# Kernel optimization log

Hardware: AMD Instinct MI355X
Metric: run time of the kernel (lower is better)

Reference implementation:

```python
import jax, jax.numpy as jnp
import numpy as np

SCALE = 8      # scale_factor from map_to_mat_info
PATCH = 32     # up_delta - low_delta + 1 == right_delta - left_delta + 1 (uniform interior patches)


def setup_inputs() -> dict:
    key = jax.random.key(0)
    mat_h, mat_w = 160, 160
    H = (mat_h - 1) * SCALE + PATCH  # 1304: deltas (0,31,0,31) -> no border clipping
    W = (mat_w - 1) * SCALE + PATCH
    x = jax.random.normal(key, (1, 3, H, W), dtype=jnp.float32)
    rgb_weight = jnp.array([0.299, 0.587, 0.114], dtype=jnp.float32).reshape(1, 3, 1, 1)
    return {"x": x, "rgb_weight": rgb_weight, "mat_h": mat_h, "mat_w": mat_w}


def reference(x, rgb_weight, mat_h, mat_w):
    P = PATCH
    # RGB -> grayscale (convert_gray branch for in_channels == 3)
    gray = jnp.sum(x * rgb_weight, axis=1)[0]  # (H, W)
    # Gather all overlapping PxP patches at stride SCALE -> (mat_h, mat_w, P, P)
    rows = (jnp.arange(mat_h) * SCALE)[:, None] + jnp.arange(P)[None, :]  # (mat_h, P)
    cols = (jnp.arange(mat_w) * SCALE)[:, None] + jnp.arange(P)[None, :]  # (mat_w, P)
    p = gray[rows.reshape(-1)].reshape(mat_h, P, -1)              # (mat_h, P, W)
    p = p[:, :, cols.reshape(-1)].reshape(mat_h, P, mat_w, P)     # (mat_h, P, mat_w, P)
    patches = jnp.transpose(p, (0, 2, 1, 3))                      # (mat_h, mat_w, P, P)
    # torch.rfft(signal_ndim=2, onesided=False) == full 2D FFT; power = re^2 + im^2
    F = jnp.fft.fft2(patches)
    log_power = jnp.log(F.real * F.real + F.imag * F.imag + 1.0)
    # High-frequency region sums (h == w == P, static)
    lo = P // 2 - P // 4 - 1   # 7
    up = P // 2 + P // 4       # 24
    r1 = jnp.sum(log_power[..., lo:up + 1, :], axis=(-2, -1))
    r2 = jnp.sum(log_power[..., up + 1:, lo:up + 1], axis=(-2, -1))
    r3 = jnp.sum(log_power[..., :lo, lo:up + 1], axis=(-2, -1))
    mat = (r1 + r2 + r3)[None, None]  # (1, 1, mat_h, mat_w)
    return mat / jnp.max(mat)
```

## Files before the change

### kernel.cpp

```cpp
#include <hip/hip_runtime.h>
#include <math.h>

#define SCALE 8
#define PSZ 32

__device__ constexpr float C32[16] = {
     1.000000000000000f,  0.980785280403230f,  0.923879532511287f,  0.831469612302545f,
     0.707106781186548f,  0.555570233019602f,  0.382683432365090f,  0.195090322016128f,
     0.000000000000000f, -0.195090322016128f, -0.382683432365090f, -0.555570233019602f,
    -0.707106781186548f, -0.831469612302545f, -0.923879532511287f, -0.980785280403230f };
__device__ constexpr float S32[16] = {
     0.000000000000000f,  0.195090322016128f,  0.382683432365090f,  0.555570233019602f,
     0.707106781186548f,  0.831469612302545f,  0.923879532511287f,  0.980785280403230f,
     1.000000000000000f,  0.980785280403230f,  0.923879532511287f,  0.831469612302545f,
     0.707106781186548f,  0.555570233019602f,  0.382683432365090f,  0.195090322016128f };

__device__ __forceinline__ constexpr int brev5(int i) {
    return ((i & 1) << 4) | ((i & 2) << 2) | (i & 4) | ((i & 8) >> 2) | ((i & 16) >> 4);
}

__device__ __forceinline__ void fft32(float re[PSZ], float im[PSZ]) {
#pragma unroll
    for (int i = 0; i < 32; ++i) {
        const int j = brev5(i);
        if (j > i) {
            float t = re[i]; re[i] = re[j]; re[j] = t;
            t = im[i]; im[i] = im[j]; im[j] = t;
        }
    }
#pragma unroll
    for (int s = 1; s <= 5; ++s) {
        const int m = 1 << s;
        const int h = m >> 1;
        const int tstep = 32 >> s;
#pragma unroll
        for (int k = 0; k < 32; k += m) {
#pragma unroll
            for (int j = 0; j < h; ++j) {
                const float wr = C32[j * tstep];
                const float wi = -S32[j * tstep];
                const int a = k + j;
                const int b = k + j + h;
                const float tr = wr * re[b] - wi * im[b];
                const float ti = wr * im[b] + wi * re[b];
                re[b] = re[a] - tr; im[b] = im[a] - ti;
                re[a] = re[a] + tr; im[a] = im[a] + ti;
            }
        }
    }
}

__device__ __forceinline__ unsigned pack_bf2(float hi, float lo) {
    const unsigned uh = __float_as_uint(hi) + 0x8000u;
    const unsigned ul = __float_as_uint(lo) + 0x8000u;
    return (uh & 0xFFFF0000u) | (ul >> 16);
}
__device__ __forceinline__ float bf_hi(unsigned u) { return __uint_as_float(u & 0xFFFF0000u); }
__device__ __forceinline__ float bf_lo(unsigned u) { return __uint_as_float(u << 16); }

__global__ __launch_bounds__(256) void gray_kernel(
        const float* __restrict__ x, const float* __restrict__ w,
        float* __restrict__ g, int n4, long long HW) {
    const int i = blockIdx.x * 256 + threadIdx.x;
    if (i >= n4) return;
    const float w0 = w[0], w1 = w[1], w2 = w[2];
    const float4 a = reinterpret_cast<const float4*>(x)[i];
    const float4 b = reinterpret_cast<const float4*>(x + HW)[i];
    const float4 c = reinterpret_cast<const float4*>(x + 2 * HW)[i];
    float4 o;
    o.x = w0 * a.x + w1 * b.x + w2 * c.x;
    o.y = w0 * a.y + w1 * b.y + w2 * c.y;
    o.z = w0 * a.z + w1 * b.z + w2 * c.z;
    o.w = w0 * a.w + w1 * b.w + w2 * c.w;
    reinterpret_cast<float4*>(g)[i] = o;
}

template <bool GRAY_PRE>
__global__ __launch_bounds__(64) void hfdft_patch_kernel(
        const float* __restrict__ x, const float* __restrict__ w,
        float* __restrict__ out, int H, int W, int mat_h, int mat_w) {
    __shared__ unsigned cb[4 * 528];

    const int lane = threadIdx.x;
    const int total = mat_h * mat_w;
    const long long HW = (long long)H * W;

    {
        const int g = lane >> 5, r = lane & 31;
        int pA = blockIdx.x * 4 + 2 * g;
        if (pA > total - 1) pA = total - 1;
        int pB = pA + 1; if (pB > total - 1) pB = total - 1;
        const int phA = pA / mat_w, pwA = pA % mat_w;
        const int phB = pB / mat_w, pwB = pB % mat_w;
        const bool adj = (phA == phB) && (pwB == pwA + 1);

        float re[PSZ], im[PSZ];
        if (GRAY_PRE) {
            if (adj) {
                const int base = (phA * SCALE + r) * W + pwA * SCALE;
                const float4* g4 = reinterpret_cast<const float4*>(x + base);
                float win[40];
#pragma unroll
                for (int q = 0; q < 10; ++q) {
                    const float4 v = g4[q];
                    win[4 * q + 0] = v.x; win[4 * q + 1] = v.y;
                    win[4 * q + 2] = v.z; win[4 * q + 3] = v.w;
                }
#pragma unroll
                for (int i = 0; i < PSZ; ++i) { re[i] = win[i]; im[i] = win[i + 8]; }
            } else {
                const int baseA = (phA * SCALE + r) * W + pwA * SCALE;
                const int baseB = (phB * SCALE + r) * W + pwB * SCALE;
#pragma unroll
                for (int i = 0; i < PSZ; ++i) { re[i] = x[baseA + i]; im[i] = x[baseB + i]; }
            }
        } else {
            const float w0 = w[0], w1 = w[1], w2 = w[2];
            if (adj && ((W & 3) == 0)) {
                const int base = (phA * SCALE + r) * W + pwA * SCALE;
                const float4* a4 = reinterpret_cast<const float4*>(x + base);
                const float4* b4 = reinterpret_cast<const float4*>(x + HW + base);
                const float4* c4 = reinterpret_cast<const float4*>(x + 2 * HW + base);
                float win[40];
#pragma unroll
                for (int q = 0; q < 10; ++q) {
                    const float4 a = a4[q], b = b4[q], c = c4[q];
                    win[4 * q + 0] = w0 * a.x + w1 * b.x + w2 * c.x;
                    win[4 * q + 1] = w0 * a.y + w1 * b.y + w2 * c.y;
                    win[4 * q + 2] = w0 * a.z + w1 * b.z + w2 * c.z;
                    win[4 * q + 3] = w0 * a.w + w1 * b.w + w2 * c.w;
                }
#pragma unroll
                for (int i = 0; i < PSZ; ++i) { re[i] = win[i]; im[i] = win[i + 8]; }
            } else {
                const int baseA = (phA * SCALE + r) * W + pwA * SCALE;
                const int baseB = (phB * SCALE + r) * W + pwB * SCALE;
#pragma unroll
                for (int i = 0; i < PSZ; ++i) {
                    re[i] = w0 * x[baseA + i] + w1 * x[HW + baseA + i] + w2 * x[2 * HW + baseA + i];
                    im[i] = w0 * x[baseB + i] + w1 * x[HW + baseB + i] + w2 * x[2 * HW + baseB + i];
                }
            }
        }

        fft32(re, im);

        unsigned* cbA = cb + (2 * g) * 528;
        unsigned* cbB = cbA + 528;
        cbA[r] = pack_bf2(re[0], re[16]);
        cbB[r] = pack_bf2(im[0], im[16]);
#pragma unroll
        for (int k = 1; k <= 15; ++k) {
            const int m = 32 - k;
            const float far_ = 0.5f * (re[k] + re[m]);
            const float fai_ = 0.5f * (im[k] - im[m]);
            const float fbr_ = 0.5f * (im[k] + im[m]);
            const float fbi_ = 0.5f * (re[m] - re[k]);
            cbA[k * 33 + r] = pack_bf2(far_, fai_);
            cbB[k * 33 + r] = pack_bf2(fbr_, fbi_);
        }
    }

    __syncthreads();

    {
        const int pl = lane >> 4, slot = lane & 15;
        const int p = blockIdx.x * 4 + pl;
        const unsigned* cbp = cb + pl * 528 + slot * 33;

        float cre[PSZ], cim[PSZ];
#pragma unroll
        for (int r2 = 0; r2 < PSZ; ++r2) {
            const unsigned u = cbp[r2];
            cre[r2] = bf_hi(u);
            cim[r2] = bf_lo(u);
        }

        fft32(cre, cim);

        float s0 = 0.0f, s1 = 0.0f;
        if (slot == 0) {
#pragma unroll
            for (int kr = 0; kr <= 16; ++kr) {
                const int m = (32 - kr) & 31;
                const float g0r = 0.5f * (cre[kr] + cre[m]);
                const float g0i = 0.5f * (cim[kr] - cim[m]);
                const float g1r = 0.5f * (cim[kr] + cim[m]);
                const float g1i = 0.5f * (cre[m] - cre[kr]);
                const float w0c = (kr >= 7 ? 1.0f : 0.0f) + ((kr >= 8 && kr <= 15) ? 1.0f : 0.0f);
                const float w16c = 1.0f + ((kr >= 1 && kr <= 15) ? 1.0f : 0.0f);
                if (w0c > 0.0f)
                    s0 = fmaf(w0c, __logf(g0r * g0r + g0i * g0i + 1.0f), s0);
                s1 = fmaf(w16c, __logf(g1r * g1r + g1i * g1i + 1.0f), s1);
            }
        } else {
            const float b1f = (slot >= 7) ? 1.0f : 0.0f;
            const float m1f = (slot >= 8) ? 1.0f : 0.0f;
#pragma unroll
            for (int kr = 0; kr < 32; ++kr) {
                const float lp = __logf(cre[kr] * cre[kr] + cim[kr] * cim[kr] + 1.0f);
                float wgt;
                if (kr >= 8 && kr <= 24)      wgt = 2.0f;
                else if (kr == 7)             wgt = 1.0f + m1f;
                else if (kr == 25)            wgt = b1f + 1.0f;
                else                          wgt = b1f + m1f;
                if (kr & 1) s1 = fmaf(wgt, lp, s1);
                else        s0 = fmaf(wgt, lp, s0);
            }
        }
        float s = s0 + s1;

#pragma unroll
        for (int off = 8; off >= 1; off >>= 1) s += __shfl_xor(s, off, 16);
        if (slot == 0 && p < total) out[p] = s;
    }
}

__global__ __launch_bounds__(1024) void max_kernel(
        const float* __restrict__ sums, int n, float* __restrict__ mx) {
    __shared__ float sm[16];
    float m = 0.0f;
    for (int i = threadIdx.x; i < n; i += 1024) m = fmaxf(m, sums[i]);
#pragma unroll
    for (int off = 32; off >= 1; off >>= 1) m = fmaxf(m, __shfl_xor(m, off, 64));
    if ((threadIdx.x & 63) == 0) sm[threadIdx.x >> 6] = m;
    __syncthreads();
    if (threadIdx.x == 0) {
#pragma unroll
        for (int i = 1; i < 16; ++i) m = fmaxf(m, sm[i]);
        mx[0] = m;
    }
}

__global__ __launch_bounds__(256) void norm_kernel(
        float* __restrict__ out, int n, const float* __restrict__ mx) {
    const int i = blockIdx.x * 256 + threadIdx.x;
    if (i < n) out[i] = out[i] / mx[0];
}

extern "C" void kernel_launch(void* const* d_in, const int* in_sizes, int n_in,
                              void* d_out, int out_size, void* d_ws, size_t ws_size,
                              hipStream_t stream) {
    const float* x = (const float*)d_in[0];
    const float* w = (const float*)d_in[1];
    float* out = (float*)d_out;

    const int HWi = in_sizes[0] / 3;
    const int H = (int)(sqrt((double)HWi) + 0.5);
    const int W = H;
    const long long HW = (long long)H * W;
    const int mat = (int)(sqrt((double)out_size) + 0.5);
    const int total = mat * mat;
    const int blocksA = (total + 3) / 4;

    float* maxbuf = (float*)d_ws;
    float* gray = (float*)((char*)d_ws + 256);
    const size_t need = 256 + (size_t)HW * 4;

    if (ws_size >= need && (W & 3) == 0) {
        const int n4 = (int)(HW / 4);
        hipLaunchKernelGGL(gray_kernel, dim3((n4 + 255) / 256), dim3(256), 0, stream,
                           x, w, gray, n4, HW);
        hipLaunchKernelGGL((hfdft_patch_kernel<true>), dim3(blocksA), dim3(64), 0, stream,
                           gray, w, out, H, W, mat, mat);
    } else {
        hipLaunchKernelGGL((hfdft_patch_kernel<false>), dim3(blocksA), dim3(64), 0, stream,
                           x, w, out, H, W, mat, mat);
    }
    hipLaunchKernelGGL(max_kernel, dim3(1), dim3(1024), 0, stream, out, total, maxbuf);
    hipLaunchKernelGGL(norm_kernel, dim3((total + 255) / 256), dim3(256), 0, stream,
                       out, total, maxbuf);
}
```

Before: 43.84 us.

## Pack two waves per FFT block, drop barrier, parallelize max with atomics

The patch FFT kernel now runs two independent 64-lane waves per block, each on its own LDS region, and swaps the block-wide barrier for an LDS waitcnt because each wave only reads what it wrote itself. The max reduction is spread over 8 blocks that combine with an unsigned atomicMax on the float bits, which is valid because the sums are non-negative. A memset is added to zero the max buffer first. This cuts barrier cost and the serial single-block reduction, at the price of an extra memset and reliance on wave-synchronous LDS behavior.

```diff
diff --git a/kernel.cpp b/kernel.cpp
--- a/kernel.cpp
+++ b/kernel.cpp
@@ -76,18 +76,22 @@
 }
 
 template <bool GRAY_PRE>
-__global__ __launch_bounds__(64) void hfdft_patch_kernel(
+__global__ __launch_bounds__(128) void hfdft_patch_kernel(
         const float* __restrict__ x, const float* __restrict__ w,
         float* __restrict__ out, int H, int W, int mat_h, int mat_w) {
-    __shared__ unsigned cb[4 * 528];
-
-    const int lane = threadIdx.x;
+    __shared__ unsigned cb[8 * 528];
+
+    const int tid = threadIdx.x;
+    const int wid = tid >> 6;
+    const int lane = tid & 63;
+    const int P0 = blockIdx.x * 8 + wid * 4;
     const int total = mat_h * mat_w;
     const long long HW = (long long)H * W;
+    unsigned* cbw = cb + wid * 4 * 528;
 
     {
         const int g = lane >> 5, r = lane & 31;
-        int pA = blockIdx.x * 4 + 2 * g;
+        int pA = P0 + 2 * g;
         if (pA > total - 1) pA = total - 1;
         int pB = pA + 1; if (pB > total - 1) pB = total - 1;
         const int phA = pA / mat_w, pwA = pA % mat_w;
@@ -145,7 +149,7 @@
 
         fft32(re, im);
 
-        unsigned* cbA = cb + (2 * g) * 528;
+        unsigned* cbA = cbw + (2 * g) * 528;
         unsigned* cbB = cbA + 528;
         cbA[r] = pack_bf2(re[0], re[16]);
         cbB[r] = pack_bf2(im[0], im[16]);
@@ -161,12 +165,12 @@
         }
     }
 
-    __syncthreads();
+    asm volatile("s_waitcnt lgkmcnt(0)" ::: "memory");
 
     {
         const int pl = lane >> 4, slot = lane & 15;
-        const int p = blockIdx.x * 4 + pl;
-        const unsigned* cbp = cb + pl * 528 + slot * 33;
+        const int p = P0 + pl;
+        const unsigned* cbp = cbw + pl * 528 + slot * 33;
 
         float cre[PSZ], cim[PSZ];
 #pragma unroll
@@ -217,10 +221,11 @@
 }
 
 __global__ __launch_bounds__(1024) void max_kernel(
-        const float* __restrict__ sums, int n, float* __restrict__ mx) {
+        const float* __restrict__ sums, int n, unsigned* __restrict__ mx) {
     __shared__ float sm[16];
     float m = 0.0f;
-    for (int i = threadIdx.x; i < n; i += 1024) m = fmaxf(m, sums[i]);
+    for (int i = blockIdx.x * 1024 + threadIdx.x; i < n; i += gridDim.x * 1024)
+        m = fmaxf(m, sums[i]);
 #pragma unroll
     for (int off = 32; off >= 1; off >>= 1) m = fmaxf(m, __shfl_xor(m, off, 64));
     if ((threadIdx.x & 63) == 0) sm[threadIdx.x >> 6] = m;
@@ -228,14 +233,14 @@
     if (threadIdx.x == 0) {
 #pragma unroll
         for (int i = 1; i < 16; ++i) m = fmaxf(m, sm[i]);
-        mx[0] = m;
+        atomicMax(mx, __float_as_uint(m));
     }
 }
 
 __global__ __launch_bounds__(256) void norm_kernel(
-        float* __restrict__ out, int n, const float* __restrict__ mx) {
+        float* __restrict__ out, int n, const unsigned* __restrict__ mx) {
     const int i = blockIdx.x * 256 + threadIdx.x;
-    if (i < n) out[i] = out[i] / mx[0];
+    if (i < n) out[i] = out[i] / __uint_as_float(mx[0]);
 }
 
 extern "C" void kernel_launch(void* const* d_in, const int* in_sizes, int n_in,
@@ -251,23 +256,25 @@
     const long long HW = (long long)H * W;
     const int mat = (int)(sqrt((double)out_size) + 0.5);
     const int total = mat * mat;
-    const int blocksA = (total + 3) / 4;
-
-    float* maxbuf = (float*)d_ws;
+    const int blocksA = (total + 7) / 8;
+
+    unsigned* maxbuf = (unsigned*)d_ws;
     float* gray = (float*)((char*)d_ws + 256);
     const size_t need = 256 + (size_t)HW * 4;
+
+    hipMemsetAsync(maxbuf, 0, 4, stream);
 
     if (ws_size >= need && (W & 3) == 0) {
         const int n4 = (int)(HW / 4);
         hipLaunchKernelGGL(gray_kernel, dim3((n4 + 255) / 256), dim3(256), 0, stream,
                            x, w, gray, n4, HW);
-        hipLaunchKernelGGL((hfdft_patch_kernel<true>), dim3(blocksA), dim3(64), 0, stream,
+        hipLaunchKernelGGL((hfdft_patch_kernel<true>), dim3(blocksA), dim3(128), 0, stream,
                            gray, w, out, H, W, mat, mat);
     } else {
-        hipLaunchKernelGGL((hfdft_patch_kernel<false>), dim3(blocksA), dim3(64), 0, stream,
+        hipLaunchKernelGGL((hfdft_patch_kernel<false>), dim3(blocksA), dim3(128), 0, stream,
                            x, w, out, H, W, mat, mat);
     }
-    hipLaunchKernelGGL(max_kernel, dim3(1), dim3(1024), 0, stream, out, total, maxbuf);
+    hipLaunchKernelGGL(max_kernel, dim3(8), dim3(1024), 0, stream, out, total, maxbuf);
     hipLaunchKernelGGL(norm_kernel, dim3((total + 255) / 256), dim3(256), 0, stream,
                        out, total, maxbuf);
 }
```

After: 47.57 us. 1.09x slower.
